# Optimization experiments

Hardware: AMD Instinct MI355X
Metric: run time of the kernel (lower is better)

## Reference

```python
import jax, jax.numpy as jnp
import numpy as np
import math

B, S, H, NH = 4, 2048, 128, 8  # batch, seq_len, hdim (== per-head dim == model dim), nheads


def setup_inputs() -> dict:
    key = jax.random.key(0)
    kx, kqkv, kproj = jax.random.split(key, 3)
    x = jax.random.normal(kx, (B, S, H), dtype=jnp.float32)
    # torch.rand -> uniform [0,1), scaled by 1/sqrt(hdim), matching the module init
    qkv = jax.random.uniform(kqkv, (H, 3 * NH * H), dtype=jnp.float32) / math.sqrt(H)
    projection = jax.random.uniform(kproj, (H * NH, H), dtype=jnp.float32) / math.sqrt(H)
    return {"x": x, "qkv": qkv, "projection": projection}


def reference(x, qkv, projection):
    b, s, h = x.shape
    nh = qkv.shape[1] // (3 * h)
    Q, K, V = jnp.split(qkv, 3, axis=1)  # each (h, nh*h)
    # NOTE: faithful to the original: raw reshape of contiguous [b, s, nh*h]
    # into [b, nh, s, h] WITHOUT a transpose (heads tile the (s, feat) layout).
    q = (x @ Q).reshape(b, nh, s, h)
    k = (x @ K).reshape(b, nh, s, h)
    v = (x @ V).reshape(b, nh, s, h)
    scale = 1.0 / math.sqrt(h)
    att = jnp.einsum("bnsh,bnth->bnst", q, k) * scale  # [b, nh, s, s]
    causal = jnp.tril(jnp.ones((s, s), dtype=bool))
    att = jnp.where(causal[None, None], att, -jnp.inf)
    att = jax.nn.softmax(att, axis=-1)
    # dropout p = 0.0 -> identity
    out = jnp.einsum("bnst,bnth->bnsh", att, v)  # [b, nh, s, h]
    out = out.reshape(b, s, nh * h)  # faithful raw reshape (matches .view(B, S, -1))
    return out @ projection  # [b, s, h]
```

## Files before the change

### kernel.cpp

```cpp
#include <hip/hip_runtime.h>
#include <math.h>

#define BATCH 4
#define SEQ   2048
#define HDIM  128
#define NHEAD 8
#define MROWS (BATCH*SEQ)
#define QKVN  (3*NHEAD*HDIM)
#define YN    (NHEAD*HDIM)

#define CS 0.12751744f

using bfrag = __attribute__((ext_vector_type(8))) short;
using f32x4 = __attribute__((ext_vector_type(4))) float;
using s16x4 = __attribute__((ext_vector_type(4))) short;

__device__ __forceinline__ f32x4 mfma16(bfrag a, bfrag b, f32x4 c) {
    return __builtin_amdgcn_mfma_f32_16x16x32_bf16(a, b, c, 0, 0, 0);
}
__device__ __forceinline__ short f2bf(float f) {
    union { float f; unsigned u; } v; v.f = f;
    unsigned r = v.u + 0x7FFFu + ((v.u >> 16) & 1u);
    return (short)(r >> 16);
}
__device__ __forceinline__ unsigned cvtpk(float lo, float hi) {
    unsigned r;
    asm("v_cvt_pk_bf16_f32 %0, %1, %2" : "=v"(r) : "v"(lo), "v"(hi));
    return r;
}
__device__ __forceinline__ void perm32swap(unsigned &x, unsigned &y) {
    asm volatile("v_permlane32_swap_b32 %0, %1" : "+v"(x), "+v"(y));
}
__device__ __forceinline__ f32x4 z4() { f32x4 z; z[0]=0.f; z[1]=0.f; z[2]=0.f; z[3]=0.f; return z; }

__device__ __forceinline__ void redist(const float p[4][4], bool hi16,
                                       bfrag &pa0o, bfrag &pa1o) {
    unsigned pk0[2], pk1[2], pk2[2], pk3[2];
    pk0[0] = cvtpk(p[0][0], p[0][1]); pk0[1] = cvtpk(p[0][2], p[0][3]);
    pk1[0] = cvtpk(p[1][0], p[1][1]); pk1[1] = cvtpk(p[1][2], p[1][3]);
    pk2[0] = cvtpk(p[2][0], p[2][1]); pk2[1] = cvtpk(p[2][2], p[2][3]);
    pk3[0] = cvtpk(p[3][0], p[3][1]); pk3[1] = cvtpk(p[3][2], p[3][3]);
    uint4 w0, w1;
    {
        unsigned A = pk0[0], C = pk1[0];
        perm32swap(A, C);
        unsigned A16 = __shfl_xor((int)A, 16), C16 = __shfl_xor((int)C, 16);
        w0.x = hi16 ? C16 : A;
        w0.z = hi16 ? C   : A16;
        unsigned B = pk0[1], D = pk1[1];
        perm32swap(B, D);
        unsigned B16 = __shfl_xor((int)B, 16), D16 = __shfl_xor((int)D, 16);
        w0.y = hi16 ? D16 : B;
        w0.w = hi16 ? D   : B16;
    }
    {
        unsigned E = pk2[0], G = pk3[0];
        perm32swap(E, G);
        unsigned E16 = __shfl_xor((int)E, 16), G16 = __shfl_xor((int)G, 16);
        w1.x = hi16 ? G16 : E;
        w1.z = hi16 ? G   : E16;
        unsigned F = pk2[1], H = pk3[1];
        perm32swap(F, H);
        unsigned F16 = __shfl_xor((int)F, 16), H16 = __shfl_xor((int)H, 16);
        w1.y = hi16 ? H16 : F;
        w1.w = hi16 ? H   : F16;
    }
    union { uint4 u; bfrag f; } cv0, cv1;
    cv0.u = w0; cv1.u = w1;
    pa0o = cv0.f; pa1o = cv1.f;
}

__global__ __launch_bounds__(256) void conv_x(const float* __restrict__ x, short* __restrict__ XB) {
    int i = (blockIdx.x * 256 + threadIdx.x) * 4;
    float4 v = *(const float4*)(x + i);
    s16x4 o; o[0] = f2bf(v.x); o[1] = f2bf(v.y); o[2] = f2bf(v.z); o[3] = f2bf(v.w);
    *(s16x4*)(XB + i) = o;
}
__global__ __launch_bounds__(256) void conv_qkvT(const float* __restrict__ q, short* __restrict__ qT) {
    int t = blockIdx.x * 256 + threadIdx.x;
    int n = t >> 7, k = t & 127;
    qT[t] = f2bf(q[(size_t)k * QKVN + n]);
}
__global__ __launch_bounds__(256) void conv_projT(const float* __restrict__ p, short* __restrict__ pT) {
    int t = blockIdx.x * 256 + threadIdx.x;
    int h = t >> 10, r = t & 1023;
    pT[t] = f2bf(p[(size_t)r * HDIM + h]);
}

__global__ __launch_bounds__(256) void gemm_qkv(
    const short* __restrict__ XB, const short* __restrict__ qkvT,
    short* __restrict__ Qh, short* __restrict__ Kh, short* __restrict__ Vh)
{
    const int t = threadIdx.x, lane = t & 63, w = t >> 6;
    const int lr = lane & 15, lg = lane >> 4;
    const int m0 = blockIdx.x * 128 + (w >> 1) * 64;
    const int n0 = blockIdx.y * 128 + (w & 1) * 64;

    f32x4 acc[4][4];
    #pragma unroll
    for (int i = 0; i < 4; ++i)
        #pragma unroll
        for (int j = 0; j < 4; ++j) acc[i][j] = z4();

    #pragma unroll
    for (int c = 0; c < 4; ++c) {
        bfrag a[4], bb[4];
        #pragma unroll
        for (int rt = 0; rt < 4; ++rt)
            a[rt] = *(const bfrag*)(XB + (size_t)(m0 + rt * 16 + lr) * 128 + c * 32 + lg * 8);
        #pragma unroll
        for (int nt = 0; nt < 4; ++nt)
            bb[nt] = *(const bfrag*)(qkvT + (size_t)(n0 + nt * 16 + lr) * 128 + c * 32 + lg * 8);
        #pragma unroll
        for (int rt = 0; rt < 4; ++rt)
            #pragma unroll
            for (int nt = 0; nt < 4; ++nt)
                acc[rt][nt] = mfma16(a[rt], bb[nt], acc[rt][nt]);
    }

    const int part = blockIdx.y >> 3, c8 = blockIdx.y & 7;
    short* dst = (part == 0) ? Qh : ((part == 1) ? Kh : Vh);
    #pragma unroll
    for (int rt = 0; rt < 4; ++rt)
        #pragma unroll
        for (int j = 0; j < 4; ++j) {
            int r = m0 + rt * 16 + lg * 4 + j;
            int b = r >> 11, sl = r & 2047;
            int n = sl >> 8, s2 = (sl & 255) * 8 + c8;
            size_t rowbase = ((size_t)((b * 8 + n) * 2048 + s2)) * 128;
            #pragma unroll
            for (int nt = 0; nt < 4; ++nt) {
                int h = (w & 1) * 64 + nt * 16 + lr;
                dst[rowbase + h] = f2bf(acc[rt][nt][j]);
            }
        }
}

__global__ __launch_bounds__(256) void transp_v(
    const short* __restrict__ Vh, short* __restrict__ Vt)
{
    __shared__ short Ls[64][72];
    const int bn = blockIdx.z, s20 = blockIdx.x * 64, d0 = blockIdx.y * 64;
    const int t = threadIdx.x;
    const short* src = Vh + ((size_t)bn * SEQ + s20) * 128 + d0;
    {
        int r = t >> 2, ch = (t & 3) * 16;
        *(int4*)&Ls[r][ch]     = *(const int4*)(src + (size_t)r * 128 + ch);
        *(int4*)&Ls[r][ch + 8] = *(const int4*)(src + (size_t)r * 128 + ch + 8);
    }
    __syncthreads();
    {
        int dr = t >> 2, ch = (t & 3) * 16;
        short tmp[16];
        #pragma unroll
        for (int i = 0; i < 16; ++i) tmp[i] = Ls[ch + i][dr];
        short* dp = Vt + ((size_t)bn * HDIM + d0 + dr) * SEQ + s20 + ch;
        *(int4*)dp       = *(int4*)&tmp[0];
        *(int4*)(dp + 8) = *(int4*)&tmp[8];
    }
}

__global__ __launch_bounds__(256) void attn10(
    const short* __restrict__ Qh, const short* __restrict__ Kh,
    const short* __restrict__ Vt, short* __restrict__ Y)
{
    __shared__ __align__(16) short Kls[2][64 * 128];
    __shared__ __align__(16) short Vls[2][128 * 64];

    const int t = threadIdx.x, lane = t & 63, w = t >> 6;
    const int lr = lane & 15, lg = lane >> 4;

    const int g  = blockIdx.x;
    const int bn = g & 31;
    const int pp = g >> 5;
    const int b  = bn >> 3, n = bn & 7;

    const short* Qb = Qh + (size_t)bn * SEQ * HDIM;
    const short* Kb = Kh + (size_t)bn * SEQ * HDIM;
    const short* Vb = Vt + (size_t)bn * HDIM * SEQ;

    auto stageK = [&](int buf, int k0) {
        #pragma unroll
        for (int i = 0; i < 4; ++i) {
            const int q = w * 4 + i;
            const int rowK = q * 4 + (lane >> 4);
            const short* src = Kb + (size_t)(k0 + rowK) * 128 + (((lane & 15) ^ (rowK & 7)) * 8);
            __builtin_amdgcn_global_load_lds(
                (const __attribute__((address_space(1))) unsigned int*)src,
                (__attribute__((address_space(3))) unsigned int*)&Kls[buf][q * 512 + lane * 8],
                16, 0, 0);
        }
    };
    auto stageV = [&](int buf, int k0) {
        #pragma unroll
        for (int i = 0; i < 4; ++i) {
            const int q = w * 4 + i;
            const int d = q * 8 + (lane >> 3);
            const short* src = Vb + (size_t)d * SEQ + k0 + (((lane & 7) ^ (d & 7)) * 8);
            __builtin_amdgcn_global_load_lds(
                (const __attribute__((address_space(1))) unsigned int*)src,
                (__attribute__((address_space(3))) unsigned int*)&Vls[buf][q * 512 + lane * 8],
                16, 0, 0);
        }
    };

    const int sw = lr & 7;
    const bool hi16 = (lg & 1);

    #pragma unroll 1
    for (int phase = 0; phase < 2; ++phase) {
        const int tile = phase ? pp : (31 - pp);
        const int q0 = tile * 64 + w * 16;

        bfrag qf[4];
        #pragma unroll
        for (int c = 0; c < 4; ++c)
            qf[c] = *(const bfrag*)(Qb + (size_t)(q0 + lr) * 128 + c * 32 + lg * 8);

        float mcs = -1.0e30f, l = 0.f;
        f32x4 o[8];
        #pragma unroll
        for (int dt = 0; dt < 8; ++dt) o[dt] = z4();

        stageV(0, 0);
        stageK(0, 0);
        __syncthreads();

        for (int s = 0; s <= tile; ++s) {
            const int cur = s & 1;
            const int k0 = s * 64;
            if (s < tile) { stageV(cur ^ 1, k0 + 64); stageK(cur ^ 1, k0 + 64); }

            f32x4 sA[4];
            #pragma unroll
            for (int kt = 0; kt < 4; ++kt) sA[kt] = z4();
            const int ktend = (s == tile) ? (w + 1) : 4;
            __builtin_amdgcn_s_setprio(1);
            #pragma unroll
            for (int kt = 0; kt < 4; ++kt) {
                if (kt < ktend) {
                    const char* kbase = (const char*)&Kls[cur][0] + (kt * 16 + lr) * 256;
                    #pragma unroll
                    for (int c = 0; c < 4; ++c) {
                        bfrag kb = *(const bfrag*)(kbase + (((c * 4 + lg) ^ sw) * 16));
                        sA[kt] = mfma16(kb, qf[c], sA[kt]);
                    }
                }
            }
            __builtin_amdgcn_s_setprio(0);

            if (s == tile) {
                #pragma unroll
                for (int kt = 0; kt < 4; ++kt)
                    #pragma unroll
                    for (int j = 0; j < 4; ++j)
                        if (kt * 16 + lg * 4 + j > w * 16 + lr)
                            sA[kt][j] = -3.0e38f;
            }

            float mx = fmaxf(fmaxf(sA[0][0], sA[0][1]), fmaxf(sA[0][2], sA[0][3]));
            #pragma unroll
            for (int kt = 1; kt < 4; ++kt)
                mx = fmaxf(mx, fmaxf(fmaxf(sA[kt][0], sA[kt][1]),
                                     fmaxf(sA[kt][2], sA[kt][3])));
            mx = fmaxf(mx, __shfl_xor(mx, 16));
            mx = fmaxf(mx, __shfl_xor(mx, 32));
            const float pmx = mx * CS;

            if (__any((pmx > mcs + 8.0f) ? 1 : 0)) {
                float nm = fmaxf(mcs, pmx);
                float al = exp2f(mcs - nm);
                mcs = nm;
                l *= al;
                float alj[4];
                #pragma unroll
                for (int j = 0; j < 4; ++j) alj[j] = __shfl(al, lg * 4 + j);
                #pragma unroll
                for (int dt = 0; dt < 8; ++dt)
                    #pragma unroll
                    for (int j = 0; j < 4; ++j) o[dt][j] *= alj[j];
            }

            float p[4][4];
            float ls = 0.f;
            #pragma unroll
            for (int kt = 0; kt < 4; ++kt)
                #pragma unroll
                for (int j = 0; j < 4; ++j) {
                    p[kt][j] = exp2f(sA[kt][j] * CS - mcs);
                    ls += p[kt][j];
                }
            ls += __shfl_xor(ls, 16);
            ls += __shfl_xor(ls, 32);
            l += ls;

            bfrag pa0, pa1;
            redist(p, hi16, pa0, pa1);

            __builtin_amdgcn_s_setprio(1);
            #pragma unroll
            for (int dt = 0; dt < 8; ++dt) {
                const char* vbase = (const char*)&Vls[cur][0] + (dt * 16 + lr) * 128;
                bfrag vb0 = *(const bfrag*)(vbase + ((lg ^ sw) * 16));
                bfrag vb1 = *(const bfrag*)(vbase + (((4 + lg) ^ sw) * 16));
                o[dt] = mfma16(pa0, vb0, o[dt]);
                o[dt] = mfma16(pa1, vb1, o[dt]);
            }
            __builtin_amdgcn_s_setprio(0);

            __syncthreads();
        }

        float inv[4];
        #pragma unroll
        for (int j = 0; j < 4; ++j) inv[j] = 1.0f / __shfl(l, lg * 4 + j);
        #pragma unroll
        for (int j = 0; j < 4; ++j) {
            int s2 = q0 + lg * 4 + j;
            size_t yrow = (size_t)b * SEQ + n * 256 + (s2 >> 3);
            short* yp = Y + yrow * YN + (s2 & 7) * 128 + lr;
            #pragma unroll
            for (int dt = 0; dt < 8; ++dt)
                yp[dt * 16] = f2bf(o[dt][j] * inv[j]);
        }
    }
}

__global__ __launch_bounds__(128) void gemm_out(
    const short* __restrict__ Yb, const short* __restrict__ projT, float* __restrict__ out)
{
    const int t = threadIdx.x, lane = t & 63, w = t >> 6;
    const int lr = lane & 15, lg = lane >> 4;
    const int m0 = blockIdx.x * 16;
    const int n0 = w * 64;

    f32x4 acc[4];
    #pragma unroll
    for (int j = 0; j < 4; ++j) acc[j] = z4();

    for (int c = 0; c < 32; ++c) {
        bfrag a = *(const bfrag*)(Yb + (size_t)(m0 + lr) * YN + c * 32 + lg * 8);
        #pragma unroll
        for (int nt = 0; nt < 4; ++nt) {
            bfrag bb = *(const bfrag*)(projT + (size_t)(n0 + nt * 16 + lr) * YN + c * 32 + lg * 8);
            acc[nt] = mfma16(a, bb, acc[nt]);
        }
    }
    #pragma unroll
    for (int nt = 0; nt < 4; ++nt)
        #pragma unroll
        for (int j = 0; j < 4; ++j)
            out[(size_t)(m0 + lg * 4 + j) * HDIM + n0 + nt * 16 + lr] = acc[nt][j];
}

extern "C" void kernel_launch(void* const* d_in, const int* in_sizes, int n_in,
                              void* d_out, int out_size, void* d_ws, size_t ws_size,
                              hipStream_t stream)
{
    const float* x    = (const float*)d_in[0];
    const float* qkv  = (const float*)d_in[1];
    const float* proj = (const float*)d_in[2];
    float* out = (float*)d_out;

    const size_t HEADSZ = (size_t)32 * SEQ * HDIM;

    short* XB    = (short*)d_ws;
    short* qkvT  = XB    + (size_t)MROWS * HDIM;
    short* projT = qkvT  + (size_t)QKVN * HDIM;
    short* Qh    = projT + (size_t)HDIM * YN;
    short* Kh    = Qh    + HEADSZ;
    short* Vh    = Kh    + HEADSZ;
    short* Vtb   = Vh    + HEADSZ;
    short* Yb    = Vtb   + HEADSZ;

    conv_x    <<<MROWS * HDIM / 1024, 256, 0, stream>>>(x, XB);
    conv_qkvT <<<QKVN * HDIM / 256,  256, 0, stream>>>(qkv, qkvT);
    conv_projT<<<HDIM * YN / 256,    256, 0, stream>>>(proj, projT);

    gemm_qkv<<<dim3(MROWS / 128, QKVN / 128), 256, 0, stream>>>(XB, qkvT, Qh, Kh, Vh);
    transp_v<<<dim3(SEQ / 64, HDIM / 64, 32), 256, 0, stream>>>(Vh, Vtb);
    attn10  <<<512, 256, 0, stream>>>(Qh, Kh, Vtb, Yb);
    gemm_out<<<MROWS / 16, 128, 0, stream>>>(Yb, projT, out);
}
```

Baseline: 146.6 us.

## Fuse x conversion and V transpose into QKV GEMM; widen output GEMM blocks

The fp32-to-bf16 conversion of x now happens inside gemm_qkv when the A fragments are loaded, so the separate conv_x kernel and its XB buffer are gone. The V slice of the QKV GEMM writes straight into the transposed Vt layout, which removes the transp_v kernel and the intermediate Vh round trip. gemm_out now runs 4 waves per block with 2 n-tiles each instead of 2 waves with 4, giving more waves per block. The risks are that each x element is converted again by every n-block, and that the transposed V stores are strided scalar writes that coalesce poorly.

After: 185.5 us. 26.6% more time.

```diff
diff --git a/kernel.cpp b/kernel.cpp
--- a/kernel.cpp
+++ b/kernel.cpp
@@ -70,12 +70,6 @@
     pa0o = cv0.f; pa1o = cv1.f;
 }
 
-__global__ __launch_bounds__(256) void conv_x(const float* __restrict__ x, short* __restrict__ XB) {
-    int i = (blockIdx.x * 256 + threadIdx.x) * 4;
-    float4 v = *(const float4*)(x + i);
-    s16x4 o; o[0] = f2bf(v.x); o[1] = f2bf(v.y); o[2] = f2bf(v.z); o[3] = f2bf(v.w);
-    *(s16x4*)(XB + i) = o;
-}
 __global__ __launch_bounds__(256) void conv_qkvT(const float* __restrict__ q, short* __restrict__ qT) {
     int t = blockIdx.x * 256 + threadIdx.x;
     int n = t >> 7, k = t & 127;
@@ -88,8 +82,8 @@
 }
 
 __global__ __launch_bounds__(256) void gemm_qkv(
-    const short* __restrict__ XB, const short* __restrict__ qkvT,
-    short* __restrict__ Qh, short* __restrict__ Kh, short* __restrict__ Vh)
+    const float* __restrict__ x, const short* __restrict__ qkvT,
+    short* __restrict__ Qh, short* __restrict__ Kh, short* __restrict__ Vt)
 {
     const int t = threadIdx.x, lane = t & 63, w = t >> 6;
     const int lr = lane & 15, lg = lane >> 4;
@@ -106,8 +100,15 @@
     for (int c = 0; c < 4; ++c) {
         bfrag a[4], bb[4];
         #pragma unroll
-        for (int rt = 0; rt < 4; ++rt)
-            a[rt] = *(const bfrag*)(XB + (size_t)(m0 + rt * 16 + lr) * 128 + c * 32 + lg * 8);
+        for (int rt = 0; rt < 4; ++rt) {
+            const float* xp = x + (size_t)(m0 + rt * 16 + lr) * 128 + c * 32 + lg * 8;
+            float4 v0 = *(const float4*)xp;
+            float4 v1 = *(const float4*)(xp + 4);
+            a[rt][0] = f2bf(v0.x); a[rt][1] = f2bf(v0.y);
+            a[rt][2] = f2bf(v0.z); a[rt][3] = f2bf(v0.w);
+            a[rt][4] = f2bf(v1.x); a[rt][5] = f2bf(v1.y);
+            a[rt][6] = f2bf(v1.z); a[rt][7] = f2bf(v1.w);
+        }
         #pragma unroll
         for (int nt = 0; nt < 4; ++nt)
             bb[nt] = *(const bfrag*)(qkvT + (size_t)(n0 + nt * 16 + lr) * 128 + c * 32 + lg * 8);
@@ -119,44 +120,37 @@
     }
 
     const int part = blockIdx.y >> 3, c8 = blockIdx.y & 7;
-    short* dst = (part == 0) ? Qh : ((part == 1) ? Kh : Vh);
-    #pragma unroll
-    for (int rt = 0; rt < 4; ++rt)
-        #pragma unroll
-        for (int j = 0; j < 4; ++j) {
-            int r = m0 + rt * 16 + lg * 4 + j;
-            int b = r >> 11, sl = r & 2047;
-            int n = sl >> 8, s2 = (sl & 255) * 8 + c8;
-            size_t rowbase = ((size_t)((b * 8 + n) * 2048 + s2)) * 128;
-            #pragma unroll
-            for (int nt = 0; nt < 4; ++nt) {
-                int h = (w & 1) * 64 + nt * 16 + lr;
-                dst[rowbase + h] = f2bf(acc[rt][nt][j]);
-            }
-        }
-}
-
-__global__ __launch_bounds__(256) void transp_v(
-    const short* __restrict__ Vh, short* __restrict__ Vt)
-{
-    __shared__ short Ls[64][72];
-    const int bn = blockIdx.z, s20 = blockIdx.x * 64, d0 = blockIdx.y * 64;
-    const int t = threadIdx.x;
-    const short* src = Vh + ((size_t)bn * SEQ + s20) * 128 + d0;
-    {
-        int r = t >> 2, ch = (t & 3) * 16;
-        *(int4*)&Ls[r][ch]     = *(const int4*)(src + (size_t)r * 128 + ch);
-        *(int4*)&Ls[r][ch + 8] = *(const int4*)(src + (size_t)r * 128 + ch + 8);
-    }
-    __syncthreads();
-    {
-        int dr = t >> 2, ch = (t & 3) * 16;
-        short tmp[16];
-        #pragma unroll
-        for (int i = 0; i < 16; ++i) tmp[i] = Ls[ch + i][dr];
-        short* dp = Vt + ((size_t)bn * HDIM + d0 + dr) * SEQ + s20 + ch;
-        *(int4*)dp       = *(int4*)&tmp[0];
-        *(int4*)(dp + 8) = *(int4*)&tmp[8];
+    if (part < 2) {
+        short* dst = part ? Kh : Qh;
+        #pragma unroll
+        for (int rt = 0; rt < 4; ++rt)
+            #pragma unroll
+            for (int j = 0; j < 4; ++j) {
+                int r = m0 + rt * 16 + lg * 4 + j;
+                int b = r >> 11, sl = r & 2047;
+                int n = sl >> 8, s2 = (sl & 255) * 8 + c8;
+                size_t rowbase = ((size_t)((b * 8 + n) * 2048 + s2)) * 128;
+                #pragma unroll
+                for (int nt = 0; nt < 4; ++nt) {
+                    int h = (w & 1) * 64 + nt * 16 + lr;
+                    dst[rowbase + h] = f2bf(acc[rt][nt][j]);
+                }
+            }
+    } else {
+        #pragma unroll
+        for (int rt = 0; rt < 4; ++rt)
+            #pragma unroll
+            for (int j = 0; j < 4; ++j) {
+                int r = m0 + rt * 16 + lg * 4 + j;
+                int b = r >> 11, sl = r & 2047;
+                int n = sl >> 8, s2 = (sl & 255) * 8 + c8;
+                size_t base = ((size_t)((b * 8 + n) * 128)) * 2048 + s2;
+                #pragma unroll
+                for (int nt = 0; nt < 4; ++nt) {
+                    int h = (w & 1) * 64 + nt * 16 + lr;
+                    Vt[base + (size_t)h * 2048] = f2bf(acc[rt][nt][j]);
+                }
+            }
     }
 }
 
@@ -326,28 +320,26 @@
     }
 }
 
-__global__ __launch_bounds__(128) void gemm_out(
+__global__ __launch_bounds__(256) void gemm_out(
     const short* __restrict__ Yb, const short* __restrict__ projT, float* __restrict__ out)
 {
     const int t = threadIdx.x, lane = t & 63, w = t >> 6;
     const int lr = lane & 15, lg = lane >> 4;
     const int m0 = blockIdx.x * 16;
-    const int n0 = w * 64;
-
-    f32x4 acc[4];
-    #pragma unroll
-    for (int j = 0; j < 4; ++j) acc[j] = z4();
+    const int n0 = w * 32;
+
+    f32x4 acc[2] = {z4(), z4()};
 
     for (int c = 0; c < 32; ++c) {
         bfrag a = *(const bfrag*)(Yb + (size_t)(m0 + lr) * YN + c * 32 + lg * 8);
         #pragma unroll
-        for (int nt = 0; nt < 4; ++nt) {
+        for (int nt = 0; nt < 2; ++nt) {
             bfrag bb = *(const bfrag*)(projT + (size_t)(n0 + nt * 16 + lr) * YN + c * 32 + lg * 8);
             acc[nt] = mfma16(a, bb, acc[nt]);
         }
     }
     #pragma unroll
-    for (int nt = 0; nt < 4; ++nt)
+    for (int nt = 0; nt < 2; ++nt)
         #pragma unroll
         for (int j = 0; j < 4; ++j)
             out[(size_t)(m0 + lg * 4 + j) * HDIM + n0 + nt * 16 + lr] = acc[nt][j];
@@ -364,21 +356,17 @@
 
     const size_t HEADSZ = (size_t)32 * SEQ * HDIM;
 
-    short* XB    = (short*)d_ws;
-    short* qkvT  = XB    + (size_t)MROWS * HDIM;
+    short* qkvT  = (short*)d_ws;
     short* projT = qkvT  + (size_t)QKVN * HDIM;
     short* Qh    = projT + (size_t)HDIM * YN;
     short* Kh    = Qh    + HEADSZ;
-    short* Vh    = Kh    + HEADSZ;
-    short* Vtb   = Vh    + HEADSZ;
+    short* Vtb   = Kh    + HEADSZ;
     short* Yb    = Vtb   + HEADSZ;
 
-    conv_x    <<<MROWS * HDIM / 1024, 256, 0, stream>>>(x, XB);
-    conv_qkvT <<<QKVN * HDIM / 256,  256, 0, stream>>>(qkv, qkvT);
-    conv_projT<<<HDIM * YN / 256,    256, 0, stream>>>(proj, projT);
-
-    gemm_qkv<<<dim3(MROWS / 128, QKVN / 128), 256, 0, stream>>>(XB, qkvT, Qh, Kh, Vh);
-    transp_v<<<dim3(SEQ / 64, HDIM / 64, 32), 256, 0, stream>>>(Vh, Vtb);
+    conv_qkvT <<<QKVN * HDIM / 256, 256, 0, stream>>>(qkv, qkvT);
+    conv_projT<<<HDIM * YN / 256,   256, 0, stream>>>(proj, projT);
+
+    gemm_qkv<<<dim3(MROWS / 128, QKVN / 128), 256, 0, stream>>>(x, qkvT, Qh, Kh, Vtb);
     attn10  <<<512, 256, 0, stream>>>(Qh, Kh, Vtb, Yb);
-    gemm_out<<<MROWS / 16, 128, 0, stream>>>(Yb, projT, out);
-}
+    gemm_out<<<MROWS / 16, 256, 0, stream>>>(Yb, projT, out);
+}
```
